# Performance work log

Measured on AMD Instinct MI355X. Metric: run time of the kernel, lower is better.

Reference implementation:

```python
import jax, jax.numpy as jnp
import numpy as np

S, H, K, B, T = 128, 512, 16, 2048, 67  # state, hidden, bm, batch(paths), len(ts)


def _lin(key, i, o):
    kw, kb = jax.random.split(key)
    w = jax.random.normal(kw, (i, o), jnp.float32) / np.sqrt(i).astype(np.float32)
    b = jax.random.normal(kb, (o,), jnp.float32) * 0.01
    return w, b


def setup_inputs() -> dict:
    key = jax.random.key(0)
    ks = jax.random.split(key, 10)
    enc_w1, enc_b1 = _lin(ks[0], 3, H)
    enc_w2, enc_b2 = _lin(ks[1], H, S)
    f_w1, f_b1 = _lin(ks[2], S + 1, H)
    f_w2, f_b2 = _lin(ks[3], H, H)
    f_w3, f_b3 = _lin(ks[4], H, S)
    g_w1, g_b1 = _lin(ks[5], S + 1, H)
    g_w2, g_b2 = _lin(ks[6], H, S * K)
    ts = jnp.linspace(0.0, 1.0, T, dtype=jnp.float32)
    x = jax.random.normal(ks[7], (B, 3), jnp.float32)
    # standard-normal Brownian increments; scaled by sqrt(dt) inside reference
    dW = jax.random.normal(ks[8], (T - 4, B, K), jnp.float32)
    return dict(ts=ts, x=x,
                enc_w1=enc_w1, enc_b1=enc_b1, enc_w2=enc_w2, enc_b2=enc_b2,
                f_w1=f_w1, f_b1=f_b1, f_w2=f_w2, f_b2=f_b2, f_w3=f_w3, f_b3=f_b3,
                g_w1=g_w1, g_b1=g_b1, g_w2=g_w2, g_b2=g_b2, dW=dW)


def reference(ts, x, enc_w1, enc_b1, enc_w2, enc_b2,
              f_w1, f_b1, f_w2, f_b2, f_w3, f_b3,
              g_w1, g_b1, g_w2, g_b2, dW):
    Bn = x.shape[0]
    Sn = enc_w2.shape[1]
    Kn = dW.shape[-1]

    # encoder: y0 = MLP(x)  -> [B, S]
    y0 = jax.nn.relu(x @ enc_w1 + enc_b1) @ enc_w2 + enc_b2

    ts_sol = ts[3:]                      # solve grid, length T-3
    dts = ts_sol[1:] - ts_sol[:-1]       # [T-4]
    dWs = dW * jnp.sqrt(dts)[:, None, None]  # Brownian increments ~ N(0, dt)

    def with_time(t, y):  # concat scalar time onto state -> [B, S+1]
        tcol = jnp.broadcast_to(jnp.reshape(t, (1, 1)), (Bn, 1)).astype(y.dtype)
        return jnp.concatenate([tcol, y], axis=-1)

    def drift(t, y):  # f(t,y): [B,S]
        h = jax.nn.relu(with_time(t, y) @ f_w1 + f_b1)
        h = jax.nn.relu(h @ f_w2 + f_b2)
        return h @ f_w3 + f_b3

    def g_prod(t, y, dw):  # g(t,y) @ dW : [B,S]
        h = jax.nn.relu(with_time(t, y) @ g_w1 + g_b1)
        g = (h @ g_w2 + g_b2).reshape(Bn, Sn, Kn)
        return jnp.einsum('bsk,bk->bs', g, dw)

    def step(y, inp):  # euler_heun (Stratonovich): Euler drift + Heun diffusion
        t, dt, dw = inp
        gp = g_prod(t, y, dw)
        gp_prime = g_prod(t, y + gp, dw)
        y1 = y + drift(t, y) * dt + 0.5 * (gp + gp_prime)
        return y1, y1

    _, ys = jax.lax.scan(step, y0, (ts_sol[:-1], dts, dWs))
    sol = jnp.concatenate([y0[None], ys], axis=0)  # [T-3, B, S]
    return sol.reshape(-1)
```

## Files before the change

kernel.cpp:

```cpp
#include <hip/hip_runtime.h>
#include <hip/hip_bf16.h>
#include <math.h>

#define B_  2048
#define S_  128
#define H_  512
#define K_  16
#define NSTEP 63

typedef __bf16 bf16x8 __attribute__((ext_vector_type(8)));
typedef float  f32x4  __attribute__((ext_vector_type(4)));
typedef unsigned short u16x8 __attribute__((ext_vector_type(8)));

static __device__ __forceinline__ void f2b2(float v, unsigned short& hi, unsigned short& lo)
{
    __hip_bfloat16 h = __float2bfloat16(v);
    float r = v - __bfloat162float(h);
    __hip_bfloat16 l = __float2bfloat16(r);
    hi = __builtin_bit_cast(unsigned short, h);
    lo = __builtin_bit_cast(unsigned short, l);
}

template<int BM,int BN,int WM,int WN>
__device__ __forceinline__ void gemm_core(
    const unsigned short* __restrict__ Ahi, const unsigned short* __restrict__ Alo, int lda,
    const unsigned short* __restrict__ Whi, const unsigned short* __restrict__ Wlo,
    int K, int rowBase, int colBase,
    f32x4 (&acc)[WM/16][WN/16])
{
    constexpr int MI = WM/16, NJ = WN/16, NWC = BN/WN;
    __shared__ unsigned short Als[2][4][BM][8];
    __shared__ unsigned short Bls[2][4][BN][8];

    const int tid = threadIdx.x;
    const int l   = tid & 63;
    const int wid = tid >> 6;
    const int wr  = wid / NWC, wc = wid % NWC;
    const int r16 = l & 15, kg = l >> 4;

    for (int k0 = 0; k0 < K; k0 += 32) {
#pragma unroll
        for (int e = 0; e < BM*4; e += 256) {
            int idx = e + tid;
            int row = idx % BM, g = idx / BM;
            size_t off = (size_t)(rowBase + row) * lda + k0 + g*8;
            *(int4*)&Als[0][g][row][0] = *(const int4*)&Ahi[off];
            *(int4*)&Als[1][g][row][0] = *(const int4*)&Alo[off];
        }
#pragma unroll
        for (int e = 0; e < BN*4; e += 256) {
            int idx = e + tid;
            int row = idx % BN, g = idx / BN;
            size_t off = (size_t)(colBase + row) * K + k0 + g*8;
            *(int4*)&Bls[0][g][row][0] = *(const int4*)&Whi[off];
            *(int4*)&Bls[1][g][row][0] = *(const int4*)&Wlo[off];
        }
        __syncthreads();

        bf16x8 ah[MI], al[MI], bh[NJ], bl[NJ];
#pragma unroll
        for (int i = 0; i < MI; ++i) {
            ah[i] = __builtin_bit_cast(bf16x8, *(const u16x8*)&Als[0][kg][wr*WM + i*16 + r16][0]);
            al[i] = __builtin_bit_cast(bf16x8, *(const u16x8*)&Als[1][kg][wr*WM + i*16 + r16][0]);
        }
#pragma unroll
        for (int j = 0; j < NJ; ++j) {
            bh[j] = __builtin_bit_cast(bf16x8, *(const u16x8*)&Bls[0][kg][wc*WN + j*16 + r16][0]);
            bl[j] = __builtin_bit_cast(bf16x8, *(const u16x8*)&Bls[1][kg][wc*WN + j*16 + r16][0]);
        }
#pragma unroll
        for (int i = 0; i < MI; ++i)
#pragma unroll
            for (int j = 0; j < NJ; ++j) {
                acc[i][j] = __builtin_amdgcn_mfma_f32_16x16x32_bf16(ah[i], bh[j], acc[i][j], 0, 0, 0);
                acc[i][j] = __builtin_amdgcn_mfma_f32_16x16x32_bf16(ah[i], bl[j], acc[i][j], 0, 0, 0);
                acc[i][j] = __builtin_amdgcn_mfma_f32_16x16x32_bf16(al[i], bh[j], acc[i][j], 0, 0, 0);
            }
        __syncthreads();
    }
}


__global__ __launch_bounds__(256) void k1_phase(
    const unsigned short* __restrict__ ycH, const unsigned short* __restrict__ ycL,
    const unsigned short* __restrict__ w1tH, const unsigned short* __restrict__ w1tL,
    const float* __restrict__ g_w1, const float* __restrict__ f_w1,
    const float* __restrict__ g_b1, const float* __restrict__ f_b1,
    const float* __restrict__ ts, int step,
    unsigned short* __restrict__ HAh, unsigned short* __restrict__ HAl)
{
    constexpr int BM=64, BN=64, WM=32, WN=32, MI=2, NJ=2, NWC=BN/WN;
    f32x4 acc[MI][NJ] = {};
    const int rowBase = blockIdx.x*BM, colBase = blockIdx.y*BN;
    gemm_core<BM,BN,WM,WN>(ycH, ycL, S_, w1tH, w1tL, S_, rowBase, colBase, acc);

    const int tid=threadIdx.x, l=tid&63, wid=tid>>6;
    const int wr=wid/NWC, wc=wid%NWC, r16=l&15, rg=l>>4;
    const float t = ts[3+step];
#pragma unroll
    for (int j=0;j<NJ;++j){
        int colj = colBase + wc*WN + j*16 + r16;
        float be = (colj < 512) ? (g_b1[colj] + t*g_w1[colj])
                                : (f_b1[colj-512] + t*f_w1[colj-512]);
#pragma unroll
        for (int i=0;i<MI;++i)
#pragma unroll
            for (int reg=0;reg<4;++reg){
                int row = rowBase + wr*WM + i*16 + rg*4 + reg;
                float v = fmaxf(acc[i][j][reg] + be, 0.f);
                unsigned short h,lo; f2b2(v,h,lo);
                size_t o = (size_t)row*1024 + colj;
                HAh[o]=h; HAl[o]=lo;
            }
    }
}

__global__ __launch_bounds__(256) void k2_phase(
    const unsigned short* __restrict__ HAh, const unsigned short* __restrict__ HAl,
    const unsigned short* __restrict__ gw2H, const unsigned short* __restrict__ gw2L,
    const unsigned short* __restrict__ fw2H, const unsigned short* __restrict__ fw2L,
    const float* __restrict__ g_b2, const float* __restrict__ f_b2,
    const float* __restrict__ y,
    const float* __restrict__ dWs,
    const float* __restrict__ ts, int step,
    float* __restrict__ gp,
    unsigned short* __restrict__ ytH, unsigned short* __restrict__ ytL,
    unsigned short* __restrict__ HBh, unsigned short* __restrict__ HBl)
{
    constexpr int BM=64, BN=128, WM=32, WN=64, MI=2, NJ=4, NWC=BN/WN;
    f32x4 acc[MI][NJ] = {};
    const int rowBase = blockIdx.x*BM;
    const int by = blockIdx.y;
    const int tid=threadIdx.x, l=tid&63, wid=tid>>6;
    const int wr=wid/NWC, wc=wid%NWC, r16=l&15, rg=l>>4;

    if (by < 16) {
        const int colBase = by*BN;
        gemm_core<BM,BN,WM,WN>(HAh, HAl, 1024, gw2H, gw2L, H_, rowBase, colBase, acc);
        const float dt = ts[4+step]-ts[3+step], sq = sqrtf(dt);
#pragma unroll
        for (int i=0;i<MI;++i)
#pragma unroll
            for (int reg=0;reg<4;++reg){
                int row = rowBase + wr*WM + i*16 + rg*4 + reg;
                float dwv = dWs[row*K_ + r16] * sq;
#pragma unroll
                for (int j=0;j<NJ;++j){
                    int colj = colBase + wc*WN + j*16;
                    float m = (acc[i][j][reg] + g_b2[colj + r16]) * dwv;
                    m += __shfl_xor(m,1); m += __shfl_xor(m,2);
                    m += __shfl_xor(m,4); m += __shfl_xor(m,8);
                    if (r16 == 0){
                        int idx = row*S_ + (colj>>4);
                        gp[idx] = m;
                        unsigned short h,lo; f2b2(y[idx] + m, h, lo);
                        ytH[idx]=h; ytL[idx]=lo;
                    }
                }
            }
    } else {
        const int colBase = (by-16)*BN;
        gemm_core<BM,BN,WM,WN>(HAh + 512, HAl + 512, 1024, fw2H, fw2L, H_, rowBase, colBase, acc);
#pragma unroll
        for (int j=0;j<NJ;++j){
            int colj = colBase + wc*WN + j*16 + r16;
            float be = f_b2[colj];
#pragma unroll
            for (int i=0;i<MI;++i)
#pragma unroll
                for (int reg=0;reg<4;++reg){
                    int row = rowBase + wr*WM + i*16 + rg*4 + reg;
                    float v = fmaxf(acc[i][j][reg] + be, 0.f);
                    unsigned short h,lo; f2b2(v,h,lo);
                    size_t o = (size_t)row*512 + colj;
                    HBh[o]=h; HBl[o]=lo;
                }
        }
    }
}

__global__ __launch_bounds__(256) void k3_phase(
    const unsigned short* __restrict__ ytH, const unsigned short* __restrict__ ytL,
    const unsigned short* __restrict__ w1tH, const unsigned short* __restrict__ w1tL,
    const float* __restrict__ g_b1, const float* __restrict__ g_w1,
    const unsigned short* __restrict__ HBh, const unsigned short* __restrict__ HBl,
    const unsigned short* __restrict__ fw3H, const unsigned short* __restrict__ fw3L,
    const float* __restrict__ f_b3,
    const float* __restrict__ ts, int step,
    unsigned short* __restrict__ HA2h, unsigned short* __restrict__ HA2l,
    float* __restrict__ drift)
{
    constexpr int BM=64, BN=64, WM=32, WN=32, MI=2, NJ=2, NWC=BN/WN;
    f32x4 acc[MI][NJ] = {};
    const int rowBase = blockIdx.x*BM;
    const int by = blockIdx.y;
    const int tid=threadIdx.x, l=tid&63, wid=tid>>6;
    const int wr=wid/NWC, wc=wid%NWC, r16=l&15, rg=l>>4;

    if (by < 8) {
        const int colBase = by*BN;
        gemm_core<BM,BN,WM,WN>(ytH, ytL, S_, w1tH, w1tL, S_, rowBase, colBase, acc);
        const float t = ts[3+step];
#pragma unroll
        for (int j=0;j<NJ;++j){
            int colj = colBase + wc*WN + j*16 + r16;
            float be = g_b1[colj] + t*g_w1[colj];
#pragma unroll
            for (int i=0;i<MI;++i)
#pragma unroll
                for (int reg=0;reg<4;++reg){
                    int row = rowBase + wr*WM + i*16 + rg*4 + reg;
                    float v = fmaxf(acc[i][j][reg] + be, 0.f);
                    unsigned short h,lo; f2b2(v,h,lo);
                    size_t o = (size_t)row*512 + colj;
                    HA2h[o]=h; HA2l[o]=lo;
                }
        }
    } else {
        const int colBase = (by-8)*BN;
        gemm_core<BM,BN,WM,WN>(HBh, HBl, H_, fw3H, fw3L, H_, rowBase, colBase, acc);
#pragma unroll
        for (int j=0;j<NJ;++j){
            int colj = colBase + wc*WN + j*16 + r16;
            float be = f_b3[colj];
#pragma unroll
            for (int i=0;i<MI;++i)
#pragma unroll
                for (int reg=0;reg<4;++reg){
                    int row = rowBase + wr*WM + i*16 + rg*4 + reg;
                    drift[row*S_ + colj] = acc[i][j][reg] + be;
                }
        }
    }
}

__global__ __launch_bounds__(256) void k4_phase(
    const unsigned short* __restrict__ HA2h, const unsigned short* __restrict__ HA2l,
    const unsigned short* __restrict__ gw2H, const unsigned short* __restrict__ gw2L,
    const float* __restrict__ g_b2,
    const float* __restrict__ y,
    const float* __restrict__ gp,
    const float* __restrict__ drift,
    const float* __restrict__ dWs,
    const float* __restrict__ ts, int step,
    float* __restrict__ y1,
    unsigned short* __restrict__ ycH, unsigned short* __restrict__ ycL)
{
    constexpr int BM=64, BN=128, WM=32, WN=64, MI=2, NJ=4, NWC=BN/WN;
    f32x4 acc[MI][NJ] = {};
    const int rowBase = blockIdx.x*BM;
    const int colBase = blockIdx.y*BN;
    gemm_core<BM,BN,WM,WN>(HA2h, HA2l, H_, gw2H, gw2L, H_, rowBase, colBase, acc);

    const int tid=threadIdx.x, l=tid&63, wid=tid>>6;
    const int wr=wid/NWC, wc=wid%NWC, r16=l&15, rg=l>>4;
    const float dt = ts[4+step]-ts[3+step], sq = sqrtf(dt);
#pragma unroll
    for (int i=0;i<MI;++i)
#pragma unroll
        for (int reg=0;reg<4;++reg){
            int row = rowBase + wr*WM + i*16 + rg*4 + reg;
            float dwv = dWs[row*K_ + r16] * sq;
#pragma unroll
            for (int j=0;j<NJ;++j){
                int colj = colBase + wc*WN + j*16;
                float m = (acc[i][j][reg] + g_b2[colj + r16]) * dwv;
                m += __shfl_xor(m,1); m += __shfl_xor(m,2);
                m += __shfl_xor(m,4); m += __shfl_xor(m,8);
                if (r16 == 0){
                    int idx = row*S_ + (colj>>4);
                    float v1 = y[idx] + drift[idx]*dt + 0.5f*(gp[idx] + m);
                    y1[idx] = v1;
                    unsigned short h,lo; f2b2(v1,h,lo);
                    ycH[idx]=h; ycL[idx]=lo;
                }
            }
        }
}

__global__ __launch_bounds__(256) void tcast_k(
    const float* __restrict__ in, int rowOff, int Kd, int N,
    unsigned short* __restrict__ outH, unsigned short* __restrict__ outL)
{
    __shared__ float tl[32][33];
    const int kb = blockIdx.x*32, nb = blockIdx.y*32;
    const int tx = threadIdx.x, ty = threadIdx.y;
    for (int r = ty; r < 32; r += 8)
        tl[r][tx] = in[(size_t)(rowOff + kb + r)*N + nb + tx];
    __syncthreads();
    for (int r = ty; r < 32; r += 8){
        unsigned short h,lo; f2b2(tl[tx][r],h,lo);
        size_t o = (size_t)(nb + r)*Kd + kb + tx;
        outH[o]=h; outL[o]=lo;
    }
}

__global__ __launch_bounds__(128) void encoder_k(
    const float* __restrict__ x,
    const float* __restrict__ w1, const float* __restrict__ b1,
    const float* __restrict__ w2, const float* __restrict__ b2,
    float* __restrict__ y0,
    unsigned short* __restrict__ ycH, unsigned short* __restrict__ ycL)
{
    int b = blockIdx.x;
    __shared__ float h[H_];
    int tid = threadIdx.x;
    float x0 = x[b*3+0], x1 = x[b*3+1], x2 = x[b*3+2];
    for (int i = tid; i < H_; i += 128)
        h[i] = fmaxf(x0*w1[i] + x1*w1[H_+i] + x2*w1[2*H_+i] + b1[i], 0.f);
    __syncthreads();
    float acc = b2[tid];
    for (int k = 0; k < H_; ++k) acc += h[k]*w2[k*S_+tid];
    size_t o = (size_t)b*S_ + tid;
    y0[o] = acc;
    unsigned short hh,ll; f2b2(acc,hh,ll);
    ycH[o]=hh; ycL[o]=ll;
}

extern "C" void kernel_launch(void* const* d_in, const int* in_sizes, int n_in,
                              void* d_out, int out_size, void* d_ws, size_t ws_size,
                              hipStream_t stream)
{
    const float* ts     = (const float*)d_in[0];
    const float* x      = (const float*)d_in[1];
    const float* enc_w1 = (const float*)d_in[2];
    const float* enc_b1 = (const float*)d_in[3];
    const float* enc_w2 = (const float*)d_in[4];
    const float* enc_b2 = (const float*)d_in[5];
    const float* f_w1   = (const float*)d_in[6];
    const float* f_b1   = (const float*)d_in[7];
    const float* f_w2   = (const float*)d_in[8];
    const float* f_b2   = (const float*)d_in[9];
    const float* f_w3   = (const float*)d_in[10];
    const float* f_b3   = (const float*)d_in[11];
    const float* g_w1   = (const float*)d_in[12];
    const float* g_b1   = (const float*)d_in[13];
    const float* g_w2   = (const float*)d_in[14];
    const float* g_b2   = (const float*)d_in[15];
    const float* dW     = (const float*)d_in[16];

    float* out = (float*)d_out;
    unsigned short* w = (unsigned short*)d_ws;

    unsigned short* w1tH  = w;
    unsigned short* w1tL  = w1tH  + 1024*128;
    unsigned short* gw2H  = w1tL  + 1024*128;
    unsigned short* gw2L  = gw2H  + 2048*512;
    unsigned short* fw2H  = gw2L  + 2048*512;
    unsigned short* fw2L  = fw2H  + 512*512;
    unsigned short* fw3H  = fw2L  + 512*512;
    unsigned short* fw3L  = fw3H  + 128*512;
    unsigned short* HAh   = fw3L  + 128*512;
    unsigned short* HAl   = HAh   + 2048*1024;
    unsigned short* HBh   = HAl   + 2048*1024;
    unsigned short* HBl   = HBh   + 2048*512;
    unsigned short* ytH   = HBl   + 2048*512;
    unsigned short* ytL   = ytH   + 2048*128;
    unsigned short* ycH   = ytL   + 2048*128;
    unsigned short* ycL   = ycH   + 2048*128;
    float* gp    = (float*)(ycL + 2048*128);
    float* drift = gp + 2048*128;
    unsigned short* HA2h = HAh;
    unsigned short* HA2l = HAl;

    dim3 tb(32,8);
    tcast_k<<<dim3(4,16),  tb, 0, stream>>>(g_w1, 1, 128, 512,  w1tH,          w1tL);
    tcast_k<<<dim3(4,16),  tb, 0, stream>>>(f_w1, 1, 128, 512,  w1tH+512*128,  w1tL+512*128);
    tcast_k<<<dim3(16,16), tb, 0, stream>>>(f_w2, 0, 512, 512,  fw2H,          fw2L);
    tcast_k<<<dim3(16,4),  tb, 0, stream>>>(f_w3, 0, 512, 128,  fw3H,          fw3L);
    tcast_k<<<dim3(16,64), tb, 0, stream>>>(g_w2, 0, 512, 2048, gw2H,          gw2L);

    encoder_k<<<B_, 128, 0, stream>>>(x, enc_w1, enc_b1, enc_w2, enc_b2, out, ycH, ycL);

    for (int step = 0; step < NSTEP; ++step) {
        const float* y   = out + (size_t)step * B_ * S_;
        float*       y1  = out + (size_t)(step+1) * B_ * S_;
        const float* dWs = dW  + (size_t)step * B_ * K_;

        k1_phase<<<dim3(32,16), 256, 0, stream>>>(ycH, ycL, w1tH, w1tL, g_w1, f_w1,
                                                  g_b1, f_b1, ts, step, HAh, HAl);
        k2_phase<<<dim3(32,20), 256, 0, stream>>>(HAh, HAl, gw2H, gw2L, fw2H, fw2L,
                                                  g_b2, f_b2, y, dWs, ts, step,
                                                  gp, ytH, ytL, HBh, HBl);
        k3_phase<<<dim3(32,10), 256, 0, stream>>>(ytH, ytL, w1tH, w1tL, g_b1, g_w1,
                                                  HBh, HBl, fw3H, fw3L, f_b3, ts, step,
                                                  HA2h, HA2l, drift);
        k4_phase<<<dim3(32,16), 256, 0, stream>>>(HA2h, HA2l, gw2H, gw2L, g_b2,
                                                  y, gp, drift, dWs, ts, step,
                                                  y1, ycH, ycL);
    }
}
```

Before: 7.383 ms.

## Use direct global-to-LDS loads, BK=64 tiles, and larger k1 tiles

Replaces register-staged global->LDS copies in the shared GEMM core with the global_load_lds builtin, which writes 16-byte chunks straight into shared memory. The K-step grows from 32 to 64, halving the barrier pairs per tile. k1 switches to 64x128 tiles with half as many blocks. This saves VGPRs and instructions on the load path, but doubles LDS per block and gives k1 fewer blocks to spread over the CUs.

```diff
diff --git a/kernel.cpp b/kernel.cpp
--- a/kernel.cpp
+++ b/kernel.cpp
@@ -21,61 +21,76 @@
     lo = __builtin_bit_cast(unsigned short, l);
 }
 
-template<int BM,int BN,int WM,int WN>
+static __device__ __forceinline__ void gl16(const unsigned short* g, unsigned short* l)
+{
+    __builtin_amdgcn_global_load_lds(
+        (const __attribute__((address_space(1))) unsigned int*)g,
+        (__attribute__((address_space(3))) unsigned int*)l, 16, 0, 0);
+}
+
+template<int BM,int BN,int BK,int WM,int WN>
 __device__ __forceinline__ void gemm_core(
+    unsigned short* lds,
     const unsigned short* __restrict__ Ahi, const unsigned short* __restrict__ Alo, int lda,
-    const unsigned short* __restrict__ Whi, const unsigned short* __restrict__ Wlo,
-    int K, int rowBase, int colBase,
-    f32x4 (&acc)[WM/16][WN/16])
+    const unsigned short* __restrict__ Whi, const unsigned short* __restrict__ Wlo, int K,
+    int rowBase, int colBase, f32x4 (&acc)[WM/16][WN/16])
 {
     constexpr int MI = WM/16, NJ = WN/16, NWC = BN/WN;
-    __shared__ unsigned short Als[2][4][BM][8];
-    __shared__ unsigned short Bls[2][4][BN][8];
-
-    const int tid = threadIdx.x;
-    const int l   = tid & 63;
+    constexpr int NT = (BM/WM)*(BN/WN)*64;
+    constexpr int ACH = BM*BK/8, BCH = BN*BK/8;
+    unsigned short* Ah = lds;
+    unsigned short* Al = lds + (size_t)ACH*8;
+    unsigned short* Bh = lds + (size_t)2*ACH*8;
+    unsigned short* Bl = lds + (size_t)2*ACH*8 + (size_t)BCH*8;
+
+    const int tid = threadIdx.x, lane = tid & 63;
     const int wid = tid >> 6;
-    const int wr  = wid / NWC, wc = wid % NWC;
-    const int r16 = l & 15, kg = l >> 4;
-
-    for (int k0 = 0; k0 < K; k0 += 32) {
-#pragma unroll
-        for (int e = 0; e < BM*4; e += 256) {
-            int idx = e + tid;
-            int row = idx % BM, g = idx / BM;
+    const int wr = wid / NWC, wc = wid % NWC;
+    const int r16 = lane & 15, kg = lane >> 4;
+    const int ubase = tid & ~63;
+
+    for (int k0 = 0; k0 < K; k0 += BK) {
+#pragma unroll
+        for (int c0 = 0; c0 < ACH; c0 += NT) {
+            int c = c0 + tid;
+            int row = c % BM, g = c / BM;
             size_t off = (size_t)(rowBase + row) * lda + k0 + g*8;
-            *(int4*)&Als[0][g][row][0] = *(const int4*)&Ahi[off];
-            *(int4*)&Als[1][g][row][0] = *(const int4*)&Alo[off];
-        }
-#pragma unroll
-        for (int e = 0; e < BN*4; e += 256) {
-            int idx = e + tid;
-            int row = idx % BN, g = idx / BN;
+            gl16(Ahi + off, Ah + (size_t)(c0 + ubase)*8);
+            gl16(Alo + off, Al + (size_t)(c0 + ubase)*8);
+        }
+#pragma unroll
+        for (int c0 = 0; c0 < BCH; c0 += NT) {
+            int c = c0 + tid;
+            int row = c % BN, g = c / BN;
             size_t off = (size_t)(colBase + row) * K + k0 + g*8;
-            *(int4*)&Bls[0][g][row][0] = *(const int4*)&Whi[off];
-            *(int4*)&Bls[1][g][row][0] = *(const int4*)&Wlo[off];
+            gl16(Whi + off, Bh + (size_t)(c0 + ubase)*8);
+            gl16(Wlo + off, Bl + (size_t)(c0 + ubase)*8);
         }
         __syncthreads();
-
-        bf16x8 ah[MI], al[MI], bh[NJ], bl[NJ];
-#pragma unroll
-        for (int i = 0; i < MI; ++i) {
-            ah[i] = __builtin_bit_cast(bf16x8, *(const u16x8*)&Als[0][kg][wr*WM + i*16 + r16][0]);
-            al[i] = __builtin_bit_cast(bf16x8, *(const u16x8*)&Als[1][kg][wr*WM + i*16 + r16][0]);
-        }
-#pragma unroll
-        for (int j = 0; j < NJ; ++j) {
-            bh[j] = __builtin_bit_cast(bf16x8, *(const u16x8*)&Bls[0][kg][wc*WN + j*16 + r16][0]);
-            bl[j] = __builtin_bit_cast(bf16x8, *(const u16x8*)&Bls[1][kg][wc*WN + j*16 + r16][0]);
-        }
-#pragma unroll
-        for (int i = 0; i < MI; ++i)
+#pragma unroll
+        for (int kk = 0; kk < BK/32; ++kk) {
+            bf16x8 ah[MI], al[MI], bh[NJ], bl[NJ];
+#pragma unroll
+            for (int i = 0; i < MI; ++i) {
+                int idx = (kk*4 + kg)*BM + wr*WM + i*16 + r16;
+                ah[i] = __builtin_bit_cast(bf16x8, *(const u16x8*)(Ah + (size_t)idx*8));
+                al[i] = __builtin_bit_cast(bf16x8, *(const u16x8*)(Al + (size_t)idx*8));
+            }
 #pragma unroll
             for (int j = 0; j < NJ; ++j) {
-                acc[i][j] = __builtin_amdgcn_mfma_f32_16x16x32_bf16(ah[i], bh[j], acc[i][j], 0, 0, 0);
-                acc[i][j] = __builtin_amdgcn_mfma_f32_16x16x32_bf16(ah[i], bl[j], acc[i][j], 0, 0, 0);
-                acc[i][j] = __builtin_amdgcn_mfma_f32_16x16x32_bf16(al[i], bh[j], acc[i][j], 0, 0, 0);
+                int idx = (kk*4 + kg)*BN + wc*WN + j*16 + r16;
+                bh[j] = __builtin_bit_cast(bf16x8, *(const u16x8*)(Bh + (size_t)idx*8));
+                bl[j] = __builtin_bit_cast(bf16x8, *(const u16x8*)(Bl + (size_t)idx*8));
             }
+#pragma unroll
+            for (int i = 0; i < MI; ++i)
+#pragma unroll
+                for (int j = 0; j < NJ; ++j) {
+                    acc[i][j] = __builtin_amdgcn_mfma_f32_16x16x32_bf16(ah[i], bh[j], acc[i][j], 0, 0, 0);
+                    acc[i][j] = __builtin_amdgcn_mfma_f32_16x16x32_bf16(ah[i], bl[j], acc[i][j], 0, 0, 0);
+                    acc[i][j] = __builtin_amdgcn_mfma_f32_16x16x32_bf16(al[i], bh[j], acc[i][j], 0, 0, 0);
+                }
+        }
         __syncthreads();
     }
 }
@@ -89,10 +104,11 @@
     const float* __restrict__ ts, int step,
     unsigned short* __restrict__ HAh, unsigned short* __restrict__ HAl)
 {
-    constexpr int BM=64, BN=64, WM=32, WN=32, MI=2, NJ=2, NWC=BN/WN;
+    constexpr int BM=64, BN=128, WM=32, WN=64, MI=2, NJ=4, NWC=BN/WN;
+    __shared__ __align__(16) unsigned short lds[(BM+BN)*64*2];
     f32x4 acc[MI][NJ] = {};
     const int rowBase = blockIdx.x*BM, colBase = blockIdx.y*BN;
-    gemm_core<BM,BN,WM,WN>(ycH, ycL, S_, w1tH, w1tL, S_, rowBase, colBase, acc);
+    gemm_core<BM,BN,64,WM,WN>(lds, ycH, ycL, S_, w1tH, w1tL, S_, rowBase, colBase, acc);
 
     const int tid=threadIdx.x, l=tid&63, wid=tid>>6;
     const int wr=wid/NWC, wc=wid%NWC, r16=l&15, rg=l>>4;
@@ -128,6 +144,7 @@
     unsigned short* __restrict__ HBh, unsigned short* __restrict__ HBl)
 {
     constexpr int BM=64, BN=128, WM=32, WN=64, MI=2, NJ=4, NWC=BN/WN;
+    __shared__ __align__(16) unsigned short lds[(BM+BN)*64*2];
     f32x4 acc[MI][NJ] = {};
     const int rowBase = blockIdx.x*BM;
     const int by = blockIdx.y;
@@ -136,7 +153,7 @@
 
     if (by < 16) {
         const int colBase = by*BN;
-        gemm_core<BM,BN,WM,WN>(HAh, HAl, 1024, gw2H, gw2L, H_, rowBase, colBase, acc);
+        gemm_core<BM,BN,64,WM,WN>(lds, HAh, HAl, 1024, gw2H, gw2L, H_, rowBase, colBase, acc);
         const float dt = ts[4+step]-ts[3+step], sq = sqrtf(dt);
 #pragma unroll
         for (int i=0;i<MI;++i)
@@ -160,7 +177,7 @@
             }
     } else {
         const int colBase = (by-16)*BN;
-        gemm_core<BM,BN,WM,WN>(HAh + 512, HAl + 512, 1024, fw2H, fw2L, H_, rowBase, colBase, acc);
+        gemm_core<BM,BN,64,WM,WN>(lds, HAh + 512, HAl + 512, 1024, fw2H, fw2L, H_, rowBase, colBase, acc);
 #pragma unroll
         for (int j=0;j<NJ;++j){
             int colj = colBase + wc*WN + j*16 + r16;
@@ -191,6 +208,7 @@
     float* __restrict__ drift)
 {
     constexpr int BM=64, BN=64, WM=32, WN=32, MI=2, NJ=2, NWC=BN/WN;
+    __shared__ __align__(16) unsigned short lds[(BM+BN)*64*2];
     f32x4 acc[MI][NJ] = {};
     const int rowBase = blockIdx.x*BM;
     const int by = blockIdx.y;
@@ -199,7 +217,7 @@
 
     if (by < 8) {
         const int colBase = by*BN;
-        gemm_core<BM,BN,WM,WN>(ytH, ytL, S_, w1tH, w1tL, S_, rowBase, colBase, acc);
+        gemm_core<BM,BN,64,WM,WN>(lds, ytH, ytL, S_, w1tH, w1tL, S_, rowBase, colBase, acc);
         const float t = ts[3+step];
 #pragma unroll
         for (int j=0;j<NJ;++j){
@@ -218,7 +236,7 @@
         }
     } else {
         const int colBase = (by-8)*BN;
-        gemm_core<BM,BN,WM,WN>(HBh, HBl, H_, fw3H, fw3L, H_, rowBase, colBase, acc);
+        gemm_core<BM,BN,64,WM,WN>(lds, HBh, HBl, H_, fw3H, fw3L, H_, rowBase, colBase, acc);
 #pragma unroll
         for (int j=0;j<NJ;++j){
             int colj = colBase + wc*WN + j*16 + r16;
@@ -247,10 +265,11 @@
     unsigned short* __restrict__ ycH, unsigned short* __restrict__ ycL)
 {
     constexpr int BM=64, BN=128, WM=32, WN=64, MI=2, NJ=4, NWC=BN/WN;
+    __shared__ __align__(16) unsigned short lds[(BM+BN)*64*2];
     f32x4 acc[MI][NJ] = {};
     const int rowBase = blockIdx.x*BM;
     const int colBase = blockIdx.y*BN;
-    gemm_core<BM,BN,WM,WN>(HA2h, HA2l, H_, gw2H, gw2L, H_, rowBase, colBase, acc);
+    gemm_core<BM,BN,64,WM,WN>(lds, HA2h, HA2l, H_, gw2H, gw2L, H_, rowBase, colBase, acc);
 
     const int tid=threadIdx.x, l=tid&63, wid=tid>>6;
     const int wr=wid/NWC, wc=wid%NWC, r16=l&15, rg=l>>4;
@@ -377,7 +396,7 @@
         float*       y1  = out + (size_t)(step+1) * B_ * S_;
         const float* dWs = dW  + (size_t)step * B_ * K_;
 
-        k1_phase<<<dim3(32,16), 256, 0, stream>>>(ycH, ycL, w1tH, w1tL, g_w1, f_w1,
+        k1_phase<<<dim3(32,8),  256, 0, stream>>>(ycH, ycL, w1tH, w1tL, g_w1, f_w1,
                                                   g_b1, f_b1, ts, step, HAh, HAl);
         k2_phase<<<dim3(32,20), 256, 0, stream>>>(HAh, HAl, gw2H, gw2L, fw2H, fw2L,
                                                   g_b2, f_b2, y, dWs, ts, step,
```

Result: no change. 7.322 ms (-0.8%).
